# Kernel tuning notes

Measured on AMD Instinct MI355X. Metric: run time of the kernel, lower is better.

## Reference

```python
import jax, jax.numpy as jnp
import numpy as np

B, S, DIN, DOUT = 4, 2048, 4096, 4096
QMAX = 127  # 2**(8-1) - 1


def setup_inputs() -> dict:
    key = jax.random.key(0)
    k_x, k_w, k_b, k_ws = jax.random.split(key, 4)
    x = jax.random.normal(k_x, (B, S, DIN), dtype=jnp.float32)
    # int8-valued weights stored as int32 (as in the torch module's .int() weight)
    weight = jax.random.randint(k_w, (DOUT, DIN), -QMAX, QMAX + 1, dtype=jnp.int32)
    bias = jax.random.randint(k_b, (DOUT,), -10, 11, dtype=jnp.int32)
    # per-input-channel weight scale, shape (out_features, 1)
    weight_scale = (jax.random.uniform(k_ws, (DOUT, 1), dtype=jnp.float32) * 0.01 + 1e-4)
    input_scale = jnp.float32(0.02)
    output_scale = jnp.float32(0.05)
    return {
        "x": x,
        "weight": weight,
        "bias": bias,
        "weight_scale": weight_scale,
        "input_scale": input_scale,
        "output_scale": output_scale,
    }


def reference(x, weight, bias, weight_scale, input_scale, output_scale):
    # fake-quantize activations: round to int grid, then dequantize back to float
    xq = jnp.round(x / input_scale).astype(jnp.int32).astype(jnp.float32) * input_scale
    # dequantize weights: (O, I)
    w = weight.astype(jnp.float32) * weight_scale
    # fp32 GEMM: [B,S,I] x [I,O] -> [B,S,O]
    ret = jnp.einsum("bsi,oi->bso", xq, w)
    ret = ret + bias.astype(jnp.float32)
    # requantize output to int grid (int32 output, as in torch .int())
    return jnp.round(ret / output_scale).astype(jnp.int32)
```

## Files before the change

kernel.cpp:

```cpp
#include <hip/hip_runtime.h>
#include <stdint.h>

#define MDIM 8192
#define KDIM 4096
#define NDIM 4096

typedef float f32x4 __attribute__((ext_vector_type(4)));
typedef __bf16 bf16x8 __attribute__((ext_vector_type(8)));
typedef short short8 __attribute__((ext_vector_type(8)));
typedef float fl4 __attribute__((ext_vector_type(4)));
typedef int i32x4 __attribute__((ext_vector_type(4)));

__device__ __forceinline__ short f2bf_bits(float f) {
    unsigned int u = __float_as_uint(f);
    u += 0x7fffu + ((u >> 16) & 1u);
    return (short)(u >> 16);
}

__device__ __forceinline__ void gload_lds16(const void* g, void* l) {
    __builtin_amdgcn_global_load_lds(
        (__attribute__((address_space(1))) void*)(uintptr_t)g,
        (__attribute__((address_space(3))) void*)(uintptr_t)l,
        16, 0, 0);
}

__global__ void __launch_bounds__(256) quant_x_kernel(const float* __restrict__ x,
                                                      short* __restrict__ xq,
                                                      const float* __restrict__ p_is) {
    const float inv_is = 1.0f / p_is[0];
    const int64_t i = ((int64_t)blockIdx.x * 256 + threadIdx.x) * 8;
    fl4 a = __builtin_nontemporal_load((const fl4*)(x + i));
    fl4 b = __builtin_nontemporal_load((const fl4*)(x + i + 4));
    short8 o;
    o[0] = f2bf_bits(rintf(a[0] * inv_is));
    o[1] = f2bf_bits(rintf(a[1] * inv_is));
    o[2] = f2bf_bits(rintf(a[2] * inv_is));
    o[3] = f2bf_bits(rintf(a[3] * inv_is));
    o[4] = f2bf_bits(rintf(b[0] * inv_is));
    o[5] = f2bf_bits(rintf(b[1] * inv_is));
    o[6] = f2bf_bits(rintf(b[2] * inv_is));
    o[7] = f2bf_bits(rintf(b[3] * inv_is));
    *(short8*)(xq + i) = o;
}

__global__ void __launch_bounds__(256) quant_w_kernel(const int* __restrict__ w,
                                                      short* __restrict__ wq) {
    const int64_t i = ((int64_t)blockIdx.x * 256 + threadIdx.x) * 8;
    i32x4 a = __builtin_nontemporal_load((const i32x4*)(w + i));
    i32x4 b = __builtin_nontemporal_load((const i32x4*)(w + i + 4));
    short8 o;
    o[0] = f2bf_bits((float)a[0]);
    o[1] = f2bf_bits((float)a[1]);
    o[2] = f2bf_bits((float)a[2]);
    o[3] = f2bf_bits((float)a[3]);
    o[4] = f2bf_bits((float)b[0]);
    o[5] = f2bf_bits((float)b[1]);
    o[6] = f2bf_bits((float)b[2]);
    o[7] = f2bf_bits((float)b[3]);
    *(short8*)(wq + i) = o;
}

__global__ void __launch_bounds__(256) gemm_bf16_kernel(
    const short* __restrict__ A,
    const short* __restrict__ Bw,
    const int* __restrict__ bias,
    const float* __restrict__ wscale,
    const float* __restrict__ p_is,
    const float* __restrict__ p_os,
    int* __restrict__ out) {
    __shared__ __align__(16) short As[128 * 32];
    __shared__ __align__(16) short Bs[128 * 32];

    const int tid  = threadIdx.x;
    const int lane = tid & 63;
    const int wave = tid >> 6;
    const int quad = lane >> 4;
    const int r16  = lane & 15;
    const int rsw  = (r16 >> 1) & 3;

    const int bid   = blockIdx.y * gridDim.x + blockIdx.x;
    const int g     = bid >> 8;
    const int n_blk = (g & 1) * 16 + (bid & 15);
    const int m_blk = (g >> 1) * 16 + ((bid >> 4) & 15);
    const int n0 = n_blk * 128;
    const int m0 = m_blk * 128;

    const int wm = (wave & 1) * 64;
    const int wn = (wave >> 1) * 64;

    const int srow   = tid >> 2;
    const int schunk = (tid & 3) ^ ((srow >> 1) & 3);
    const short* gA0 = A  + (int64_t)(m0 + srow) * KDIM + schunk * 8;
    const short* gB0 = Bw + (int64_t)(n0 + srow) * KDIM + schunk * 8;

    short* lA0 = As + wave * 512;
    short* lA1 = As + 2048 + wave * 512;
    short* lB0 = Bs + wave * 512;
    short* lB1 = Bs + 2048 + wave * 512;

    f32x4 acc[4][4];
#pragma unroll
    for (int i = 0; i < 4; ++i)
#pragma unroll
        for (int j = 0; j < 4; ++j) acc[i][j] = (f32x4)0.0f;

    for (int k0 = 0; k0 < KDIM; k0 += 32) {
        __syncthreads();
        gload_lds16(gA0 + k0, lA0);
        gload_lds16(gA0 + k0 + 64 * KDIM, lA1);
        gload_lds16(gB0 + k0, lB0);
        gload_lds16(gB0 + k0 + 64 * KDIM, lB1);
        __syncthreads();

        bf16x8 af[4], bfr[4];
#pragma unroll
        for (int mi = 0; mi < 4; ++mi)
            af[mi] = *(const bf16x8*)(As + (wm + mi * 16 + r16) * 32 + (quad ^ rsw) * 8);
#pragma unroll
        for (int ni = 0; ni < 4; ++ni)
            bfr[ni] = *(const bf16x8*)(Bs + (wn + ni * 16 + r16) * 32 + (quad ^ rsw) * 8);

#pragma unroll
        for (int mi = 0; mi < 4; ++mi)
#pragma unroll
            for (int ni = 0; ni < 4; ++ni)
                acc[mi][ni] = __builtin_amdgcn_mfma_f32_16x16x32_bf16(
                    af[mi], bfr[ni], acc[mi][ni], 0, 0, 0);
    }

    const float is = p_is[0];
    const float inv_os = 1.0f / p_os[0];

    float alpha[4], beta[4];
#pragma unroll
    for (int ni = 0; ni < 4; ++ni) {
        const int col = n0 + wn + ni * 16 + r16;
        alpha[ni] = is * wscale[col] * inv_os;
        beta[ni]  = (float)bias[col] * inv_os;
    }

#pragma unroll
    for (int mi = 0; mi < 4; ++mi) {
        const int row0 = m0 + wm + mi * 16 + quad * 4;
#pragma unroll
        for (int ni = 0; ni < 4; ++ni) {
            const int col = n0 + wn + ni * 16 + r16;
#pragma unroll
            for (int reg = 0; reg < 4; ++reg) {
                const float v = acc[mi][ni][reg] * alpha[ni] + beta[ni];
                __builtin_nontemporal_store(__float2int_rn(v),
                                            out + (int64_t)(row0 + reg) * NDIM + col);
            }
        }
    }
}

extern "C" void kernel_launch(void* const* d_in, const int* in_sizes, int n_in,
                              void* d_out, int out_size, void* d_ws, size_t ws_size,
                              hipStream_t stream) {
    (void)in_sizes; (void)n_in; (void)out_size; (void)ws_size;
    const float* x      = (const float*)d_in[0];
    const int*   weight = (const int*)d_in[1];
    const int*   bias   = (const int*)d_in[2];
    const float* wscale = (const float*)d_in[3];
    const float* p_is   = (const float*)d_in[4];
    const float* p_os   = (const float*)d_in[5];

    short* xq = (short*)d_ws;
    short* wq = xq + (size_t)MDIM * KDIM;

    quant_x_kernel<<<(int)(((int64_t)MDIM * KDIM) / 2048), 256, 0, stream>>>(x, xq, p_is);
    quant_w_kernel<<<(int)(((int64_t)NDIM * KDIM) / 2048), 256, 0, stream>>>(weight, wq);

    dim3 grid(NDIM / 128, MDIM / 128);
    gemm_bf16_kernel<<<grid, 256, 0, stream>>>(xq, wq, bias, wscale, p_is, p_os, (int*)d_out);
}
```

Before: 555.2 us.

## Rewrite GEMM as 256x256 tile, 8-wave, double-buffered pipelined kernel with grid-stride quant

The GEMM moves from 128x128 tiles with BK=32 and two syncs per step to 256x256 tiles with BK=64, 512 threads, a 128KB double-buffered LDS, and a hand-scheduled ping-pong that overlaps global-to-LDS loads with MFMA phases using setprio and waitcnt barriers. This aims to raise arithmetic intensity and hide load latency. The quant kernels become grid-stride loops with a fixed 2048 blocks. Risks include lower occupancy from the large LDS footprint and fewer blocks (512), and fragile manual waitcnt ordering. The block-swizzle for L2 locality is also dropped.

```diff
diff --git a/kernel.cpp b/kernel.cpp
--- a/kernel.cpp
+++ b/kernel.cpp
@@ -4,6 +4,8 @@
 #define MDIM 8192
 #define KDIM 4096
 #define NDIM 4096
+#define BK   64
+#define NKT  (KDIM / BK)
 
 typedef float f32x4 __attribute__((ext_vector_type(4)));
 typedef __bf16 bf16x8 __attribute__((ext_vector_type(8)));
@@ -28,39 +30,66 @@
                                                       short* __restrict__ xq,
                                                       const float* __restrict__ p_is) {
     const float inv_is = 1.0f / p_is[0];
-    const int64_t i = ((int64_t)blockIdx.x * 256 + threadIdx.x) * 8;
-    fl4 a = __builtin_nontemporal_load((const fl4*)(x + i));
-    fl4 b = __builtin_nontemporal_load((const fl4*)(x + i + 4));
-    short8 o;
-    o[0] = f2bf_bits(rintf(a[0] * inv_is));
-    o[1] = f2bf_bits(rintf(a[1] * inv_is));
-    o[2] = f2bf_bits(rintf(a[2] * inv_is));
-    o[3] = f2bf_bits(rintf(a[3] * inv_is));
-    o[4] = f2bf_bits(rintf(b[0] * inv_is));
-    o[5] = f2bf_bits(rintf(b[1] * inv_is));
-    o[6] = f2bf_bits(rintf(b[2] * inv_is));
-    o[7] = f2bf_bits(rintf(b[3] * inv_is));
-    *(short8*)(xq + i) = o;
+    const int64_t stride = (int64_t)gridDim.x * 256 * 8;
+    for (int64_t i = ((int64_t)blockIdx.x * 256 + threadIdx.x) * 8;
+         i < (int64_t)MDIM * KDIM; i += stride) {
+        fl4 a = __builtin_nontemporal_load((const fl4*)(x + i));
+        fl4 b = __builtin_nontemporal_load((const fl4*)(x + i + 4));
+        short8 o;
+        o[0] = f2bf_bits(rintf(a[0] * inv_is));
+        o[1] = f2bf_bits(rintf(a[1] * inv_is));
+        o[2] = f2bf_bits(rintf(a[2] * inv_is));
+        o[3] = f2bf_bits(rintf(a[3] * inv_is));
+        o[4] = f2bf_bits(rintf(b[0] * inv_is));
+        o[5] = f2bf_bits(rintf(b[1] * inv_is));
+        o[6] = f2bf_bits(rintf(b[2] * inv_is));
+        o[7] = f2bf_bits(rintf(b[3] * inv_is));
+        *(short8*)(xq + i) = o;
+    }
 }
 
 __global__ void __launch_bounds__(256) quant_w_kernel(const int* __restrict__ w,
                                                       short* __restrict__ wq) {
-    const int64_t i = ((int64_t)blockIdx.x * 256 + threadIdx.x) * 8;
-    i32x4 a = __builtin_nontemporal_load((const i32x4*)(w + i));
-    i32x4 b = __builtin_nontemporal_load((const i32x4*)(w + i + 4));
-    short8 o;
-    o[0] = f2bf_bits((float)a[0]);
-    o[1] = f2bf_bits((float)a[1]);
-    o[2] = f2bf_bits((float)a[2]);
-    o[3] = f2bf_bits((float)a[3]);
-    o[4] = f2bf_bits((float)b[0]);
-    o[5] = f2bf_bits((float)b[1]);
-    o[6] = f2bf_bits((float)b[2]);
-    o[7] = f2bf_bits((float)b[3]);
-    *(short8*)(wq + i) = o;
-}
-
-__global__ void __launch_bounds__(256) gemm_bf16_kernel(
+    const int64_t stride = (int64_t)gridDim.x * 256 * 8;
+    for (int64_t i = ((int64_t)blockIdx.x * 256 + threadIdx.x) * 8;
+         i < (int64_t)NDIM * KDIM; i += stride) {
+        i32x4 a = __builtin_nontemporal_load((const i32x4*)(w + i));
+        i32x4 b = __builtin_nontemporal_load((const i32x4*)(w + i + 4));
+        short8 o;
+        o[0] = f2bf_bits((float)a[0]);
+        o[1] = f2bf_bits((float)a[1]);
+        o[2] = f2bf_bits((float)a[2]);
+        o[3] = f2bf_bits((float)a[3]);
+        o[4] = f2bf_bits((float)b[0]);
+        o[5] = f2bf_bits((float)b[1]);
+        o[6] = f2bf_bits((float)b[2]);
+        o[7] = f2bf_bits((float)b[3]);
+        *(short8*)(wq + i) = o;
+    }
+}
+
+
+#define PH_MID() do { \
+    __builtin_amdgcn_s_barrier(); \
+    asm volatile("s_waitcnt lgkmcnt(0)" ::: "memory"); \
+    __builtin_amdgcn_sched_barrier(0); \
+    __builtin_amdgcn_s_setprio(1); \
+  } while (0)
+
+#define PH_END() do { \
+    __builtin_amdgcn_s_setprio(0); \
+    __builtin_amdgcn_s_barrier(); \
+    __builtin_amdgcn_sched_barrier(0); \
+  } while (0)
+
+#define PH_END_VM() do { \
+    __builtin_amdgcn_s_setprio(0); \
+    asm volatile("s_waitcnt vmcnt(4)" ::: "memory"); \
+    __builtin_amdgcn_s_barrier(); \
+    __builtin_amdgcn_sched_barrier(0); \
+  } while (0)
+
+__global__ void __launch_bounds__(512, 2) gemm_bf16_kernel(
     const short* __restrict__ A,
     const short* __restrict__ Bw,
     const int* __restrict__ bias,
@@ -68,86 +97,130 @@
     const float* __restrict__ p_is,
     const float* __restrict__ p_os,
     int* __restrict__ out) {
-    __shared__ __align__(16) short As[128 * 32];
-    __shared__ __align__(16) short Bs[128 * 32];
+    __shared__ __align__(16) short lds[65536];
 
     const int tid  = threadIdx.x;
     const int lane = tid & 63;
     const int wave = tid >> 6;
     const int quad = lane >> 4;
     const int r16  = lane & 15;
-    const int rsw  = (r16 >> 1) & 3;
-
-    const int bid   = blockIdx.y * gridDim.x + blockIdx.x;
-    const int g     = bid >> 8;
-    const int n_blk = (g & 1) * 16 + (bid & 15);
-    const int m_blk = (g >> 1) * 16 + ((bid >> 4) & 15);
-    const int n0 = n_blk * 128;
-    const int m0 = m_blk * 128;
-
-    const int wm = (wave & 1) * 64;
-    const int wn = (wave >> 1) * 64;
-
-    const int srow   = tid >> 2;
-    const int schunk = (tid & 3) ^ ((srow >> 1) & 3);
-    const short* gA0 = A  + (int64_t)(m0 + srow) * KDIM + schunk * 8;
-    const short* gB0 = Bw + (int64_t)(n0 + srow) * KDIM + schunk * 8;
-
-    short* lA0 = As + wave * 512;
-    short* lA1 = As + 2048 + wave * 512;
-    short* lB0 = Bs + wave * 512;
-    short* lB1 = Bs + 2048 + wave * 512;
-
-    f32x4 acc[4][4];
-#pragma unroll
-    for (int i = 0; i < 4; ++i)
+    const int sw   = r16 & 7;
+
+    const int n0 = blockIdx.x * 256;
+    const int m0 = blockIdx.y * 256;
+
+    const int wmi = wave >> 2;
+    const int wni = wave & 3;
+
+    const int srow = tid >> 3;
+    const int skc  = (tid & 7) ^ (srow & 7);
+    const short* gA = A  + (int64_t)(m0 + srow) * KDIM + skc * 8;
+    const short* gB = Bw + (int64_t)(n0 + srow) * KDIM + skc * 8;
+
+#define STAGE_A(b, ha, T) do { \
+    const short* _g = gA + (int64_t)((ha) * 128) * KDIM + (T) * BK; \
+    gload_lds16(_g,             &lds[(b)*16384 + (ha)*8192 + wave*512]); \
+    gload_lds16(_g + 64*KDIM,   &lds[(b)*16384 + (ha)*8192 + 4096 + wave*512]); \
+  } while (0)
+#define STAGE_B(b, ha, T) do { \
+    const short* _g = gB + (int64_t)((ha) * 128) * KDIM + (T) * BK; \
+    gload_lds16(_g,             &lds[32768 + (b)*16384 + (ha)*8192 + wave*512]); \
+    gload_lds16(_g + 64*KDIM,   &lds[32768 + (b)*16384 + (ha)*8192 + 4096 + wave*512]); \
+  } while (0)
+
+    const int aRowOff = (wmi * 128 + r16) * 64;
+    const int bRowOff = 32768 + (wni * 64 + r16) * 64;
+    const int cOff0   = (quad ^ sw) * 8;
+    const int cOff1   = cOff0 ^ 32;
+
+#define LDA(b, mh, mi, ks) \
+    (*(const bf16x8*)&lds[(b)*16384 + aRowOff + ((mh)*64 + (mi)*16)*64 + ((ks) ? cOff1 : cOff0)])
+#define LDB(b, nh, nj, ks) \
+    (*(const bf16x8*)&lds[(b)*16384 + bRowOff + ((nh)*32 + (nj)*16)*64 + ((ks) ? cOff1 : cOff0)])
+
+#define READ_A(b, mh) do { \
+    _Pragma("unroll") for (int mi = 0; mi < 4; ++mi) { \
+        aR[mi][0] = LDA(b, mh, mi, 0); aR[mi][1] = LDA(b, mh, mi, 1); } \
+  } while (0)
+#define READ_B(b, nh, dst) do { \
+    _Pragma("unroll") for (int nj = 0; nj < 2; ++nj) { \
+        dst[nj][0] = LDB(b, nh, nj, 0); dst[nj][1] = LDB(b, nh, nj, 1); } \
+  } while (0)
+#define MFMA_Q(mh, nh, bsrc) do { \
+    _Pragma("unroll") for (int mi = 0; mi < 4; ++mi) \
+    _Pragma("unroll") for (int nj = 0; nj < 2; ++nj) \
+    _Pragma("unroll") for (int ks = 0; ks < 2; ++ks) \
+        acc[(mh)*4 + mi][(nh)*2 + nj] = __builtin_amdgcn_mfma_f32_16x16x32_bf16( \
+            aR[mi][ks], bsrc[nj][ks], acc[(mh)*4 + mi][(nh)*2 + nj], 0, 0, 0); \
+  } while (0)
+
+    f32x4 acc[8][4];
+#pragma unroll
+    for (int i = 0; i < 8; ++i)
 #pragma unroll
         for (int j = 0; j < 4; ++j) acc[i][j] = (f32x4)0.0f;
 
-    for (int k0 = 0; k0 < KDIM; k0 += 32) {
-        __syncthreads();
-        gload_lds16(gA0 + k0, lA0);
-        gload_lds16(gA0 + k0 + 64 * KDIM, lA1);
-        gload_lds16(gB0 + k0, lB0);
-        gload_lds16(gB0 + k0 + 64 * KDIM, lB1);
-        __syncthreads();
-
-        bf16x8 af[4], bfr[4];
-#pragma unroll
-        for (int mi = 0; mi < 4; ++mi)
-            af[mi] = *(const bf16x8*)(As + (wm + mi * 16 + r16) * 32 + (quad ^ rsw) * 8);
-#pragma unroll
-        for (int ni = 0; ni < 4; ++ni)
-            bfr[ni] = *(const bf16x8*)(Bs + (wn + ni * 16 + r16) * 32 + (quad ^ rsw) * 8);
-
-#pragma unroll
-        for (int mi = 0; mi < 4; ++mi)
-#pragma unroll
-            for (int ni = 0; ni < 4; ++ni)
-                acc[mi][ni] = __builtin_amdgcn_mfma_f32_16x16x32_bf16(
-                    af[mi], bfr[ni], acc[mi][ni], 0, 0, 0);
+    bf16x8 aR[4][2], bLo[2][2], bHi[2][2];
+
+    STAGE_A(0, 0, 0); STAGE_A(0, 1, 0);
+    STAGE_B(0, 0, 0); STAGE_B(0, 1, 0);
+    STAGE_B(1, 0, 1); STAGE_B(1, 1, 1);
+    asm volatile("s_waitcnt vmcnt(4)" ::: "memory");
+    __builtin_amdgcn_s_barrier();
+    __builtin_amdgcn_sched_barrier(0);
+
+    for (int it = 0; it < NKT / 2; ++it) {
+        const int t1 = 2 * it + 1;
+        const int tA = (2 * it + 2) & (NKT - 1);
+        const int tB = (2 * it + 3) & (NKT - 1);
+
+        READ_A(0, 0); READ_B(0, 0, bLo);
+        STAGE_A(1, 0, t1);
+        asm volatile("s_waitcnt lgkmcnt(8)" ::: "memory");
+        PH_MID(); MFMA_Q(0, 0, bLo); PH_END();
+        READ_B(0, 1, bHi);
+        STAGE_A(1, 1, t1);
+        PH_MID(); MFMA_Q(0, 1, bHi); PH_END();
+        READ_A(0, 1);
+        STAGE_B(0, 0, tA);
+        PH_MID(); MFMA_Q(1, 1, bHi); PH_END();
+        STAGE_B(0, 1, tA);
+        PH_MID(); MFMA_Q(1, 0, bLo); PH_END_VM();
+        READ_A(1, 0); READ_B(1, 0, bLo);
+        STAGE_A(0, 0, tA);
+        asm volatile("s_waitcnt lgkmcnt(8)" ::: "memory");
+        PH_MID(); MFMA_Q(0, 0, bLo); PH_END();
+        READ_B(1, 1, bHi);
+        STAGE_A(0, 1, tA);
+        PH_MID(); MFMA_Q(0, 1, bHi); PH_END();
+        READ_A(1, 1);
+        STAGE_B(1, 0, tB);
+        PH_MID(); MFMA_Q(1, 1, bHi); PH_END();
+        STAGE_B(1, 1, tB);
+        PH_MID(); MFMA_Q(1, 0, bLo); PH_END_VM();
     }
 
     const float is = p_is[0];
     const float inv_os = 1.0f / p_os[0];
+    const int colBase = n0 + wni * 64;
 
     float alpha[4], beta[4];
 #pragma unroll
-    for (int ni = 0; ni < 4; ++ni) {
-        const int col = n0 + wn + ni * 16 + r16;
-        alpha[ni] = is * wscale[col] * inv_os;
-        beta[ni]  = (float)bias[col] * inv_os;
-    }
-
-#pragma unroll
-    for (int mi = 0; mi < 4; ++mi) {
-        const int row0 = m0 + wm + mi * 16 + quad * 4;
-#pragma unroll
-        for (int ni = 0; ni < 4; ++ni) {
-            const int col = n0 + wn + ni * 16 + r16;
+    for (int nj = 0; nj < 4; ++nj) {
+        const int col = colBase + nj * 16 + r16;
+        alpha[nj] = is * wscale[col] * inv_os;
+        beta[nj]  = (float)bias[col] * inv_os;
+    }
+
+#pragma unroll
+    for (int mi = 0; mi < 8; ++mi) {
+        const int row0 = m0 + wmi * 128 + mi * 16 + quad * 4;
+#pragma unroll
+        for (int nj = 0; nj < 4; ++nj) {
+            const int col = colBase + nj * 16 + r16;
 #pragma unroll
             for (int reg = 0; reg < 4; ++reg) {
-                const float v = acc[mi][ni][reg] * alpha[ni] + beta[ni];
+                const float v = acc[mi][nj][reg] * alpha[nj] + beta[nj];
                 __builtin_nontemporal_store(__float2int_rn(v),
                                             out + (int64_t)(row0 + reg) * NDIM + col);
             }
@@ -169,9 +242,9 @@
     short* xq = (short*)d_ws;
     short* wq = xq + (size_t)MDIM * KDIM;
 
-    quant_x_kernel<<<(int)(((int64_t)MDIM * KDIM) / 2048), 256, 0, stream>>>(x, xq, p_is);
-    quant_w_kernel<<<(int)(((int64_t)NDIM * KDIM) / 2048), 256, 0, stream>>>(weight, wq);
-
-    dim3 grid(NDIM / 128, MDIM / 128);
-    gemm_bf16_kernel<<<grid, 256, 0, stream>>>(xq, wq, bias, wscale, p_is, p_os, (int*)d_out);
-}
+    quant_x_kernel<<<2048, 256, 0, stream>>>(x, xq, p_is);
+    quant_w_kernel<<<2048, 256, 0, stream>>>(weight, wq);
+
+    dim3 grid(NDIM / 256, MDIM / 256);
+    gemm_bf16_kernel<<<grid, 512, 0, stream>>>(xq, wq, bias, wscale, p_is, p_os, (int*)d_out);
+}
```

Measured after the change: 468.3 us. -15.7%, faster.
